# Kernel tuning notes

Measured on AMD Instinct MI355X. Metric: run time of the kernel, lower is better.

## Reference

```python
import jax, jax.numpy as jnp
import numpy as np


def hadamard_transform(x):
    """Normalized fast Walsh-Hadamard transform along the last axis.

    Equivalent to x @ H_n / sqrt(n) with H_n the Sylvester Hadamard matrix.
    Last dim must be a power of two. Computed in fp32 (rotate_fp32=True).
    """
    orig_dtype = x.dtype
    x = x.astype(jnp.float32)
    n = x.shape[-1]
    lead = x.shape[:-1]
    x = x.reshape(-1, n)  # (B, n)
    h = 1
    while h < n:
        # butterfly stage: pairs separated by h
        x = x.reshape(-1, n // (2 * h), 2, h)
        a = x[:, :, 0, :]
        b = x[:, :, 1, :]
        x = jnp.stack([a + b, a - b], axis=2).reshape(-1, n)
        h *= 2
    x = x * (1.0 / np.sqrt(n)).astype(np.float32)
    return x.reshape(lead + (n,)).astype(orig_dtype)


def setup_inputs() -> dict:
    key = jax.random.key(0)
    k1, k2, k3 = jax.random.split(key, 3)
    B, S, D_IN, D_OUT = 4, 2048, 8192, 2048
    x = jax.random.normal(k1, (B, S, D_IN), dtype=jnp.float32)
    # nn.Linear params: weight (out, in), bias (out,) with kaiming-ish scale
    W = jax.random.normal(k2, (D_OUT, D_IN), dtype=jnp.float32) * (1.0 / np.sqrt(D_IN))
    b = jax.random.normal(k3, (D_OUT,), dtype=jnp.float32) * 0.01
    return {"x": x, "W": W, "b": b}


def reference(x, W, b):
    xh = hadamard_transform(x)                      # (B, S, D_in)
    return jnp.einsum('bsd,od->bso', xh, W) + b     # (B, S, D_out)
```

## Files before the change

### kernel.cpp

```cpp
#include <hip/hip_runtime.h>
#include <hip/hip_bf16.h>
#include <stdint.h>


#define M_TOTAL 8192
#define K_TOTAL 8192
#define N_TOTAL 2048
#define D_IN 8192

typedef __attribute__((ext_vector_type(8))) short short8;
typedef __attribute__((ext_vector_type(4))) float f32x4;

typedef __attribute__((address_space(1))) void void_g;
typedef __attribute__((address_space(3))) void void_l;
typedef __attribute__((address_space(3))) short lds_s3;

__device__ __forceinline__ short f2bf(float f) {
  __hip_bfloat16 h = __float2bfloat16(f);
  return *reinterpret_cast<short*>(&h);
}

__global__ void cvt_x_kernel(const float* __restrict__ x, short* __restrict__ xb, long n) {
  long stride = (long)gridDim.x * blockDim.x * 8;
  for (long i = ((long)blockIdx.x * blockDim.x + threadIdx.x) * 8; i < n; i += stride) {
    float4 v0 = *(const float4*)(x + i);
    float4 v1 = *(const float4*)(x + i + 4);
    short8 o;
    o[0] = f2bf(v0.x); o[1] = f2bf(v0.y); o[2] = f2bf(v0.z); o[3] = f2bf(v0.w);
    o[4] = f2bf(v1.x); o[5] = f2bf(v1.y); o[6] = f2bf(v1.z); o[7] = f2bf(v1.w);
    *(short8*)(xb + i) = o;
  }
}

__global__ void fwht_w_kernel(const float* __restrict__ W, short* __restrict__ Wh) {
  __shared__ float buf[D_IN];
  const int row = blockIdx.x;
  const float* src = W + (long)row * D_IN;
  for (int i = threadIdx.x; i < D_IN / 4; i += blockDim.x)
    ((float4*)buf)[i] = ((const float4*)src)[i];
  for (int h = 1; h < D_IN; h <<= 1) {
    __syncthreads();
    for (int p = threadIdx.x; p < D_IN / 2; p += blockDim.x) {
      int i = ((p & ~(h - 1)) << 1) | (p & (h - 1));
      float a = buf[i], b = buf[i + h];
      buf[i] = a + b;
      buf[i + h] = a - b;
    }
  }
  __syncthreads();
  const float s = 0.011048543456039806f;
  short* dst = Wh + (long)row * D_IN;
  for (int i = threadIdx.x; i < D_IN; i += blockDim.x)
    dst[i] = f2bf(buf[i] * s);
}

#define NKT 256

#define ABUF(b) ((b) * 8192)
#define BBUF(b) (32768 + (b) * 8192)

#define SBAR __builtin_amdgcn_sched_barrier(0)
#define BAR __builtin_amdgcn_s_barrier()
#define FEN4 do { SBAR; asm volatile("s_waitcnt vmcnt(4)"); BAR; } while (0)
#define FEN0 do { SBAR; asm volatile("s_waitcnt vmcnt(0)"); BAR; } while (0)
#define FNOP do { } while (0)

#define STAGET(PB, KOFF)                                                                          \
  __builtin_amdgcn_global_load_lds((void_g*)(aLo + (KOFF)),                                       \
                                   (void_l*)&lds[ABUF(PB) + sdst], 16, 0, 0);                     \
  __builtin_amdgcn_global_load_lds((void_g*)(aHi + (KOFF)),                                       \
                                   (void_l*)&lds[ABUF(PB) + sdst + 4096], 16, 0, 0);              \
  __builtin_amdgcn_global_load_lds((void_g*)(bLo + (KOFF)),                                       \
                                   (void_l*)&lds[BBUF(PB) + sdst], 16, 0, 0);                     \
  __builtin_amdgcn_global_load_lds((void_g*)(bHi + (KOFF)),                                       \
                                   (void_l*)&lds[BBUF(PB) + sdst + 4096], 16, 0, 0);

#define DSR(dst, ADDR, IMM)                                                                       \
  asm volatile("ds_read_b128 %0, %1 offset:%2" : "=v"(dst) : "v"(ADDR), "i"(IMM))

#define RD_AM03(NB)                                                                               \
  DSR(am[0], aAdr, (NB) * 16384 + 0);    DSR(am[1], aAdr, (NB) * 16384 + 1024);                   \
  DSR(am[2], aAdr, (NB) * 16384 + 2048); DSR(am[3], aAdr, (NB) * 16384 + 3072);
#define RD_BN(NB)                                                                                 \
  DSR(bn[0], bAdr, (NB) * 16384 + 0);    DSR(bn[1], bAdr, (NB) * 16384 + 1024);                   \
  DSR(bn[2], bAdr, (NB) * 16384 + 2048); DSR(bn[3], bAdr, (NB) * 16384 + 3072);
#define RD_AM47(NB)                                                                               \
  DSR(am[4], aAdr, (NB) * 16384 + 4096); DSR(am[5], aAdr, (NB) * 16384 + 5120);                   \
  DSR(am[6], aAdr, (NB) * 16384 + 6144); DSR(am[7], aAdr, (NB) * 16384 + 7168);

#define MFQ(MIB)                                                                                  \
  __builtin_amdgcn_s_setprio(1);                                                                  \
  _Pragma("unroll") for (int mi = 0; mi < 4; ++mi) {                                              \
    _Pragma("unroll") for (int nj = 0; nj < 4; ++nj)                                              \
        acc[(MIB) + mi][nj] = __builtin_amdgcn_mfma_f32_16x16x32_bf16(                            \
            am[(MIB) + mi], bn[nj], acc[(MIB) + mi][nj], 0, 0, 0);                                \
  }                                                                                               \
  __builtin_amdgcn_s_setprio(0);

#define KT(DOSTG, PB, KOFF, DOPRE, NB, FEN)                                                       \
  {                                                                                               \
    asm volatile("s_waitcnt lgkmcnt(4)");                                                         \
    SBAR;                                                                                         \
    MFQ(0);                                                                                       \
    SBAR;                                                                                         \
    if (DOSTG) { STAGET(PB, KOFF); }                                                              \
    if (DOPRE) { RD_AM03(NB); }                                                                   \
    SBAR;                                                                                         \
    if (DOPRE) { asm volatile("s_waitcnt lgkmcnt(4)"); }                                          \
    else       { asm volatile("s_waitcnt lgkmcnt(0)"); }                                          \
    SBAR;                                                                                         \
    MFQ(4);                                                                                       \
    SBAR;                                                                                         \
    if (DOPRE) { RD_BN(NB); RD_AM47(NB); }                                                        \
    SBAR;                                                                                        \
    FEN;                                                                                          \
  }

__global__ __launch_bounds__(512, 2) void gemm_kernel(const short* __restrict__ A,
                                                      const short* __restrict__ B,
                                                      const float* __restrict__ bias,
                                                      float* __restrict__ C) {
  __shared__ __attribute__((aligned(16))) short lds[65536];

  const int tid = threadIdx.x;
  const int l = tid & 63;
  const int w = tid >> 6;
  const int wm = w >> 2;
  const int wn = w & 3;

  const int bid = blockIdx.x;
  const int swz = (bid & 7) * 32 + (bid >> 3);
  const int bm = swz >> 3;
  const int bn_ = swz & 7;
  const long tileM = (long)bm * 256;
  const long tileN = (long)bn_ * 256;

  const int kx = (((l >> 4) ^ ((l >> 1) & 3)) * 8);
  const int rb = (l & 15) * 32;
  const unsigned ldsbase = (unsigned)(uintptr_t)(lds_s3*)&lds[0];
  const unsigned aAdr = ldsbase + (unsigned)(wm * 4096 + rb + kx) * 2u;
  const unsigned bAdr = ldsbase + (unsigned)(32768 + wn * 2048 + rb + kx) * 2u;

  const int sdst = tid * 8;
  const int sslot = ((tid & 3) ^ ((tid >> 3) & 3)) * 8;
  const short* aLo = A + (tileM + (tid >> 2)) * (long)K_TOTAL + sslot;
  const short* aHi = aLo + 128 * (long)K_TOTAL;
  const short* bLo = B + (tileN + (tid >> 2)) * (long)K_TOTAL + sslot;
  const short* bHi = bLo + 128 * (long)K_TOTAL;

  f32x4 acc[8][4];
#pragma unroll
  for (int mi = 0; mi < 8; ++mi)
#pragma unroll
    for (int nj = 0; nj < 4; ++nj)
      acc[mi][nj] = (f32x4){0.f, 0.f, 0.f, 0.f};

  short8 am[8], bn[4];

  STAGET(0, 0);
  STAGET(1, 32);
  STAGET(2, 64);
  SBAR;
  asm volatile("s_waitcnt vmcnt(4)");
  BAR;
  RD_AM03(0);
  RD_BN(0);
  RD_AM47(0);
  SBAR;

  for (int t4 = 0; t4 < 252; t4 += 4) {
    KT(true, 3, (t4 + 3) * 32, true, 1, FEN4);
    KT(true, 0, (t4 + 4) * 32, true, 2, FEN4);
    KT(true, 1, (t4 + 5) * 32, true, 3, FEN4);
    KT(true, 2, (t4 + 6) * 32, true, 0, FEN4);
  }
  KT(true, 3, 255 * 32, true, 1, FEN4);
  KT(false, 0, 0, true, 2, FEN0);
  KT(false, 0, 0, true, 3, FNOP);
  KT(false, 0, 0, false, 0, FNOP);

  const int rb0 = (int)tileM + wm * 128 + (l >> 4) * 4;
  const int cb = (int)tileN + wn * 64 + (l & 15);
#pragma unroll
  for (int mi = 0; mi < 8; ++mi)
#pragma unroll
    for (int nj = 0; nj < 4; ++nj) {
      float bv = bias[cb + nj * 16];
      const int r0 = rb0 + mi * 16;
#pragma unroll
      for (int r = 0; r < 4; ++r)
        C[(long)(r0 + r) * N_TOTAL + cb + nj * 16] = acc[mi][nj][r] + bv;
    }
}

extern "C" void kernel_launch(void* const* d_in, const int* in_sizes, int n_in,
                              void* d_out, int out_size, void* d_ws, size_t ws_size,
                              hipStream_t stream) {
  const float* x = (const float*)d_in[0];
  const float* W = (const float*)d_in[1];
  const float* bias = (const float*)d_in[2];
  float* out = (float*)d_out;

  short* xb = (short*)d_ws;
  short* wh = (short*)((char*)d_ws + (size_t)M_TOTAL * K_TOTAL * 2);

  cvt_x_kernel<<<2048, 256, 0, stream>>>(x, xb, (long)M_TOTAL * K_TOTAL);
  fwht_w_kernel<<<N_TOTAL, 256, 0, stream>>>(W, wh);

  const int grid = (M_TOTAL / 256) * (N_TOTAL / 256);
  gemm_kernel<<<grid, 512, 0, stream>>>(xb, wh, bias, out);
}
```

Baseline: 363.0 us.

## Deepen GEMM LDS pipeline to five stages and barrier every other K-tile

Grows the shared-memory ring from four to five K-tile stages (160KB of LDS) and prefetches one more tile ahead. With the extra slack, the waitcnt-plus-barrier fence now runs only every second K-tile, which halves the number of workgroup barriers in the main loop. LDS read bases are split into low and high address registers so the immediate offsets still fit. The main loop is unrolled by ten, and the prologue and epilogue are reworked to match. The cost is higher LDS usage, which leaves no room for a second block per CU, and a more intricate hazard schedule.

```diff
diff --git a/kernel.cpp b/kernel.cpp
--- a/kernel.cpp
+++ b/kernel.cpp
@@ -57,7 +57,7 @@
 #define NKT 256
 
 #define ABUF(b) ((b) * 8192)
-#define BBUF(b) (32768 + (b) * 8192)
+#define BBUF(b) (40960 + (b) * 8192)
 
 #define SBAR __builtin_amdgcn_sched_barrier(0)
 #define BAR __builtin_amdgcn_s_barrier()
@@ -78,15 +78,19 @@
 #define DSR(dst, ADDR, IMM)                                                                       \
   asm volatile("ds_read_b128 %0, %1 offset:%2" : "=v"(dst) : "v"(ADDR), "i"(IMM))
 
+#define ABASE(NB) ((NB) < 3 ? aAdLo : aAdHi)
+#define BBASE(NB) ((NB) < 3 ? bAdLo : bAdHi)
+#define BIMM(NB)  ((((NB) < 3 ? (NB) : (NB) - 3)) * 16384)
+
 #define RD_AM03(NB)                                                                               \
-  DSR(am[0], aAdr, (NB) * 16384 + 0);    DSR(am[1], aAdr, (NB) * 16384 + 1024);                   \
-  DSR(am[2], aAdr, (NB) * 16384 + 2048); DSR(am[3], aAdr, (NB) * 16384 + 3072);
+  DSR(am[0], ABASE(NB), BIMM(NB) + 0);    DSR(am[1], ABASE(NB), BIMM(NB) + 1024);                 \
+  DSR(am[2], ABASE(NB), BIMM(NB) + 2048); DSR(am[3], ABASE(NB), BIMM(NB) + 3072);
 #define RD_BN(NB)                                                                                 \
-  DSR(bn[0], bAdr, (NB) * 16384 + 0);    DSR(bn[1], bAdr, (NB) * 16384 + 1024);                   \
-  DSR(bn[2], bAdr, (NB) * 16384 + 2048); DSR(bn[3], bAdr, (NB) * 16384 + 3072);
+  DSR(bn[0], BBASE(NB), BIMM(NB) + 0);    DSR(bn[1], BBASE(NB), BIMM(NB) + 1024);                 \
+  DSR(bn[2], BBASE(NB), BIMM(NB) + 2048); DSR(bn[3], BBASE(NB), BIMM(NB) + 3072);
 #define RD_AM47(NB)                                                                               \
-  DSR(am[4], aAdr, (NB) * 16384 + 4096); DSR(am[5], aAdr, (NB) * 16384 + 5120);                   \
-  DSR(am[6], aAdr, (NB) * 16384 + 6144); DSR(am[7], aAdr, (NB) * 16384 + 7168);
+  DSR(am[4], ABASE(NB), BIMM(NB) + 4096); DSR(am[5], ABASE(NB), BIMM(NB) + 5120);                 \
+  DSR(am[6], ABASE(NB), BIMM(NB) + 6144); DSR(am[7], ABASE(NB), BIMM(NB) + 7168);
 
 #define MFQ(MIB)                                                                                  \
   __builtin_amdgcn_s_setprio(1);                                                                  \
@@ -112,7 +116,7 @@
     MFQ(4);                                                                                       \
     SBAR;                                                                                         \
     if (DOPRE) { RD_BN(NB); RD_AM47(NB); }                                                        \
-    SBAR;                                                                                        \
+    SBAR;                                                                                         \
     FEN;                                                                                          \
   }
 
@@ -120,7 +124,7 @@
                                                       const short* __restrict__ B,
                                                       const float* __restrict__ bias,
                                                       float* __restrict__ C) {
-  __shared__ __attribute__((aligned(16))) short lds[65536];
+  __shared__ __attribute__((aligned(16))) short lds[81920];
 
   const int tid = threadIdx.x;
   const int l = tid & 63;
@@ -138,8 +142,10 @@
   const int kx = (((l >> 4) ^ ((l >> 1) & 3)) * 8);
   const int rb = (l & 15) * 32;
   const unsigned ldsbase = (unsigned)(uintptr_t)(lds_s3*)&lds[0];
-  const unsigned aAdr = ldsbase + (unsigned)(wm * 4096 + rb + kx) * 2u;
-  const unsigned bAdr = ldsbase + (unsigned)(32768 + wn * 2048 + rb + kx) * 2u;
+  const unsigned aAdLo = ldsbase + (unsigned)(wm * 4096 + rb + kx) * 2u;
+  const unsigned aAdHi = aAdLo + 49152u;
+  const unsigned bAdLo = ldsbase + 81920u + (unsigned)(wn * 2048 + rb + kx) * 2u;
+  const unsigned bAdHi = bAdLo + 49152u;
 
   const int sdst = tid * 8;
   const int sslot = ((tid & 3) ^ ((tid >> 3) & 3)) * 8;
@@ -160,6 +166,7 @@
   STAGET(0, 0);
   STAGET(1, 32);
   STAGET(2, 64);
+  STAGET(3, 96);
   SBAR;
   asm volatile("s_waitcnt vmcnt(4)");
   BAR;
@@ -168,15 +175,23 @@
   RD_AM47(0);
   SBAR;
 
-  for (int t4 = 0; t4 < 252; t4 += 4) {
-    KT(true, 3, (t4 + 3) * 32, true, 1, FEN4);
-    KT(true, 0, (t4 + 4) * 32, true, 2, FEN4);
-    KT(true, 1, (t4 + 5) * 32, true, 3, FEN4);
-    KT(true, 2, (t4 + 6) * 32, true, 0, FEN4);
-  }
-  KT(true, 3, 255 * 32, true, 1, FEN4);
-  KT(false, 0, 0, true, 2, FEN0);
+  for (int t0 = 0; t0 < 250; t0 += 10) {
+    KT(true, 4, (t0 + 4) * 32, true, 1, FNOP);
+    KT(true, 0, (t0 + 5) * 32, true, 2, FEN4);
+    KT(true, 1, (t0 + 6) * 32, true, 3, FNOP);
+    KT(true, 2, (t0 + 7) * 32, true, 4, FEN4);
+    KT(true, 3, (t0 + 8) * 32, true, 0, FNOP);
+    KT(true, 4, (t0 + 9) * 32, true, 1, FEN4);
+    KT(true, 0, (t0 + 10) * 32, true, 2, FNOP);
+    KT(true, 1, (t0 + 11) * 32, true, 3, FEN4);
+    KT(true, 2, (t0 + 12) * 32, true, 4, FNOP);
+    KT(true, 3, (t0 + 13) * 32, true, 0, FEN4);
+  }
+  KT(true, 4, 254 * 32, true, 1, FNOP);
+  KT(true, 0, 255 * 32, true, 2, FEN4);
   KT(false, 0, 0, true, 3, FNOP);
+  KT(false, 0, 0, true, 4, FEN0);
+  KT(false, 0, 0, true, 0, FNOP);
   KT(false, 0, 0, false, 0, FNOP);
 
   const int rb0 = (int)tileM + wm * 128 + (l >> 4) * 4;
```

New measurement: 357.6 us. About the same (-1.5%).
